# Kernel tuning notes

Measured on AMD Instinct MI355X. Metric: run time of the kernel, lower is better.

The kernel has to match this reference:

```python
import jax, jax.numpy as jnp
import numpy as np

B, S, E, L, H, FF, CB = 16, 1000, 512, 4, 8, 2048, 4096
DH = E // H

def _ln(x, g, b):
    m = x.mean(-1, keepdims=True)
    v = ((x - m) ** 2).mean(-1, keepdims=True)
    return (x - m) / jnp.sqrt(v + 1e-5) * g + b

def setup_inputs() -> dict:
    key = jax.random.key(0)
    cnt = [0]
    def rn(shape, s=0.02):
        cnt[0] += 1
        return jax.random.normal(jax.random.fold_in(key, cnt[0]), shape, jnp.float32) * s
    inp = {}
    inp['noisy_tokens'] = jax.random.randint(jax.random.fold_in(key, 999), (B, S), 0, CB, dtype=jnp.int32)
    inp['codebook'] = rn((CB, E), 1.0)
    # sinusoidal positional encoding, as in _create_positional_encoding
    pe = np.zeros((S, E), np.float32)
    pos = np.arange(S, dtype=np.float32)[:, None]
    div = np.exp(np.arange(0, E, 2, dtype=np.float32) * (-np.log(10000.0) / E))
    pe[:, 0::2] = np.sin(pos * div)
    pe[:, 1::2] = np.cos(pos * div)
    inp['pos_enc'] = jnp.asarray(pe)[None]  # [1,S,E]
    # transformer encoder layers (stacked over L)
    inp['qkv_w'] = rn((L, 3 * E, E)); inp['qkv_b'] = jnp.zeros((L, 3 * E))
    inp['out_w'] = rn((L, E, E));     inp['out_b'] = jnp.zeros((L, E))
    inp['ln1_g'] = jnp.ones((L, E));  inp['ln1_b'] = jnp.zeros((L, E))
    inp['ln2_g'] = jnp.ones((L, E));  inp['ln2_b'] = jnp.zeros((L, E))
    inp['ff1_w'] = rn((L, FF, E));    inp['ff1_b'] = jnp.zeros((L, FF))
    inp['ff2_w'] = rn((L, E, FF));    inp['ff2_b'] = jnp.zeros((L, E))
    inp['fin_g'] = jnp.ones((E,));    inp['fin_b'] = jnp.zeros((E,))
    # post_process: Linear, LN, GELU, Linear
    inp['pp1_w'] = rn((E, E)); inp['pp1_b'] = jnp.zeros((E,))
    inp['pp_ln_g'] = jnp.ones((E,)); inp['pp_ln_b'] = jnp.zeros((E,))
    inp['pp2_w'] = rn((E, E)); inp['pp2_b'] = jnp.zeros((E,))
    inp['res_w'] = jnp.float32(0.1)
    # feature_to_codebook: Linear, LN, GELU, Linear (codebook_dim == E)
    inp['fc1_w'] = rn((E, E)); inp['fc1_b'] = jnp.zeros((E,))
    inp['fc_ln_g'] = jnp.ones((E,)); inp['fc_ln_b'] = jnp.zeros((E,))
    inp['fc2_w'] = rn((E, E)); inp['fc2_b'] = jnp.zeros((E,))
    return inp

def reference(noisy_tokens, codebook, pos_enc, qkv_w, qkv_b, out_w, out_b,
              ln1_g, ln1_b, ln2_g, ln2_b, ff1_w, ff1_b, ff2_w, ff2_b,
              fin_g, fin_b, pp1_w, pp1_b, pp_ln_g, pp_ln_b, pp2_w, pp2_b,
              res_w, fc1_w, fc1_b, fc_ln_g, fc_ln_b, fc2_w, fc2_b):
    gelu = lambda z: jax.nn.gelu(z, approximate=False)
    # token embedding (codebook_projection is Identity) + positional encoding
    x = codebook[noisy_tokens] + pos_enc            # [B,S,E]
    # pre-norm transformer encoder (dropout=0 / eval)
    y = x
    for l in range(L):
        h = _ln(y, ln1_g[l], ln1_b[l])
        qkv = h @ qkv_w[l].T + qkv_b[l]             # [B,S,3E]
        q, k, v = jnp.split(qkv, 3, axis=-1)
        q = q.reshape(B, S, H, DH); k = k.reshape(B, S, H, DH); v = v.reshape(B, S, H, DH)
        scores = jnp.einsum('bqhd,bkhd->bhqk', q, k) / jnp.sqrt(jnp.float32(DH))
        attn = jax.nn.softmax(scores, axis=-1)
        ctx = jnp.einsum('bhqk,bkhd->bqhd', attn, v).reshape(B, S, E)
        y = y + (ctx @ out_w[l].T + out_b[l])
        h2 = _ln(y, ln2_g[l], ln2_b[l])
        y = y + (gelu(h2 @ ff1_w[l].T + ff1_b[l]) @ ff2_w[l].T + ff2_b[l])
    y = _ln(y, fin_g, fin_b)
    # post_process + residual
    pp = gelu(_ln(y @ pp1_w.T + pp1_b, pp_ln_g, pp_ln_b)) @ pp2_w.T + pp2_b
    enhanced = x + res_w * pp
    # feature_to_codebook
    fc = gelu(_ln(enhanced @ fc1_w.T + fc1_b, fc_ln_g, fc_ln_b)) @ fc2_w.T + fc2_b  # [B,S,E]
    # quantize: nearest neighbour in codebook (cdist + argmin)
    flat = fc.reshape(-1, E)
    d2 = (jnp.sum(flat ** 2, -1, keepdims=True)
          - 2.0 * flat @ codebook.T
          + jnp.sum(codebook ** 2, -1))            # [B*S, CB]
    tokens = jnp.argmin(d2, axis=-1).reshape(B, S)
    return fc, tokens
```

## Files before the change

### kernel.cpp

```cpp
#include <hip/hip_runtime.h>
#include <hip/hip_bf16.h>
#include <math.h>

#define NTOK 16000
#define E    512
#define FFD  2048
#define CBN  4096
#define SEQ  1000
#define NH   8
#define VLD  1008

typedef __hip_bfloat16 bf16;
typedef __attribute__((ext_vector_type(8))) short short8;
typedef __attribute__((ext_vector_type(4))) float f32x4;

__device__ __forceinline__ float gelu_f(float v) {
    return 0.5f * v * (1.0f + erff(v * 0.70710678118654752f));
}

__device__ __forceinline__ void split_store(float v, bf16* hi, bf16* lo, size_t idx) {
    bf16 h = __float2bfloat16(v);
    hi[idx] = h;
    lo[idx] = __float2bfloat16(v - __bfloat162float(h));
}

__device__ __forceinline__ void gll16(const bf16* g, short* l) {
    __builtin_amdgcn_global_load_lds((const __attribute__((address_space(1))) void*)g,
                                     (__attribute__((address_space(3))) void*)l, 16, 0, 0);
}

__device__ __forceinline__ void t2_ins(float v, int c, float& v1, int& c1, float& v2, int& c2) {
    const bool b1 = (v < v1) || (v == v1 && c < c1);
    const bool b2 = (v < v2) || (v == v2 && c < c2);
    if (b1) { v2 = v1; c2 = c1; v1 = v; c1 = c; }
    else if (b2) { v2 = v; c2 = c; }
}

__global__ __launch_bounds__(128) void embed_kernel(const int* __restrict__ tok,
                                                    const float* __restrict__ cb,
                                                    const float* __restrict__ pe,
                                                    float* __restrict__ y) {
    const int row = blockIdx.x;
    const int s = row % SEQ;
    const int t = tok[row];
    const int c = threadIdx.x * 4;
    const float4 cv = *(const float4*)(cb + (size_t)t * E + c);
    const float4 pv = *(const float4*)(pe + (size_t)s * E + c);
    *(float4*)(y + (size_t)row * E + c) =
        make_float4(cv.x + pv.x, cv.y + pv.y, cv.z + pv.z, cv.w + pv.w);
}

__global__ __launch_bounds__(256) void split_w(const float* __restrict__ src, int ld,
                                               int cols_log2, int n,
                                               bf16* __restrict__ hi, bf16* __restrict__ lo) {
    const int i = blockIdx.x * 256 + threadIdx.x;
    if (i >= n) return;
    const int r = i >> cols_log2;
    const int c = i & ((1 << cols_log2) - 1);
    const float v = src[(size_t)r * ld + c];
    split_store(v, hi, lo, i);
}

template<int GELU>
__global__ __launch_bounds__(256) void ln_planes(const float* __restrict__ in,
                                                 bf16* __restrict__ hi, bf16* __restrict__ lo,
                                                 const float* __restrict__ g,
                                                 const float* __restrict__ b) {
    const int lane = threadIdx.x & 63;
    const int row = blockIdx.x * 4 + (threadIdx.x >> 6);
    const float* p = in + (size_t)row * E;
    const float4 v0 = *(const float4*)(p + lane * 4);
    const float4 v1 = *(const float4*)(p + 256 + lane * 4);
    float sum = v0.x + v0.y + v0.z + v0.w + v1.x + v1.y + v1.z + v1.w;
    float sq = v0.x * v0.x + v0.y * v0.y + v0.z * v0.z + v0.w * v0.w
             + v1.x * v1.x + v1.y * v1.y + v1.z * v1.z + v1.w * v1.w;
#pragma unroll
    for (int m = 1; m < 64; m <<= 1) {
        sum += __shfl_xor(sum, m);
        sq += __shfl_xor(sq, m);
    }
    const float mean = sum * (1.0f / 512.0f);
    const float var = sq * (1.0f / 512.0f) - mean * mean;
    const float rstd = rsqrtf(var + 1e-5f);
    const float4 g0 = *(const float4*)(g + lane * 4);
    const float4 g1 = *(const float4*)(g + 256 + lane * 4);
    const float4 b0 = *(const float4*)(b + lane * 4);
    const float4 b1 = *(const float4*)(b + 256 + lane * 4);
    const size_t base = (size_t)row * E;
    float o;
    const float vv0[4] = {v0.x, v0.y, v0.z, v0.w};
    const float gg0[4] = {g0.x, g0.y, g0.z, g0.w};
    const float bb0[4] = {b0.x, b0.y, b0.z, b0.w};
    const float vv1[4] = {v1.x, v1.y, v1.z, v1.w};
    const float gg1[4] = {g1.x, g1.y, g1.z, g1.w};
    const float bb1[4] = {b1.x, b1.y, b1.z, b1.w};
#pragma unroll
    for (int t = 0; t < 4; ++t) {
        o = (vv0[t] - mean) * rstd * gg0[t] + bb0[t];
        if (GELU) o = gelu_f(o);
        split_store(o, hi, lo, base + lane * 4 + t);
        o = (vv1[t] - mean) * rstd * gg1[t] + bb1[t];
        if (GELU) o = gelu_f(o);
        split_store(o, hi, lo, base + 256 + lane * 4 + t);
    }
}

template<int OUT>
__global__ __launch_bounds__(256) void gemm_split(
    const bf16* __restrict__ Ah, const bf16* __restrict__ Al, int lda,
    const bf16* __restrict__ Wh, const bf16* __restrict__ Wl, int ldw,
    const float* __restrict__ bias,
    float* __restrict__ C, int ldc,
    bf16* __restrict__ Ohi, bf16* __restrict__ Olo, int ldp,
    const int* __restrict__ noisy, const float* __restrict__ cb,
    const float* __restrict__ pe, const float* __restrict__ resw,
    int K) {
    __shared__ __align__(16) short SB[2][4][128][32];
    const int tid = threadIdx.x;
    const int rowBase = blockIdx.y * 128;
    const int colBase = blockIdx.x * 128;
    const int wave = tid >> 6, lane = tid & 63;
    const int wm = (wave & 1) * 64, wn = (wave >> 1) * 64;
    const int lm = lane & 15;
    const int psl8 = ((lane >> 4) ^ ((lm >> 1) & 3)) * 8;

    const bf16* src = (wave == 0) ? Ah : (wave == 1) ? Al : (wave == 2) ? Wh : Wl;
    const int sld = (wave < 2) ? lda : ldw;
    const int srb = (wave < 2) ? rowBase : colBase;
    const int sslot = (lane & 3) ^ ((lane >> 3) & 3);
    const bf16* sp = src + (size_t)(srb + (lane >> 2)) * sld + sslot * 8;
    short* lb0 = &SB[0][wave][0][0];
    short* lb1 = &SB[1][wave][0][0];

    f32x4 acc[4][4];
#pragma unroll
    for (int i = 0; i < 4; ++i)
#pragma unroll
        for (int j = 0; j < 4; ++j)
            acc[i][j] = (f32x4){0.f, 0.f, 0.f, 0.f};

    const int nt = K >> 5;
    {
#pragma unroll
        for (int j = 0; j < 8; ++j)
            gll16(sp + (size_t)j * 16 * sld, lb0 + j * 512);
    }
    __syncthreads();
    int cur = 0;
    for (int t = 0; t < nt; ++t) {
        if (t + 1 < nt) {
            short* lb = cur ? lb0 : lb1;
            const bf16* p = sp + (t + 1) * 32;
#pragma unroll
            for (int j = 0; j < 8; ++j)
                gll16(p + (size_t)j * 16 * sld, lb + j * 512);
        }
        const short (*P)[128][32] = SB[cur];
        short8 ah[4], al[4], wh[4], wl[4];
#pragma unroll
        for (int i = 0; i < 4; ++i) {
            ah[i] = *(const short8*)&P[0][wm + i * 16 + lm][psl8];
            al[i] = *(const short8*)&P[1][wm + i * 16 + lm][psl8];
            wh[i] = *(const short8*)&P[2][wn + i * 16 + lm][psl8];
            wl[i] = *(const short8*)&P[3][wn + i * 16 + lm][psl8];
        }
#pragma unroll
        for (int i = 0; i < 4; ++i)
#pragma unroll
            for (int j = 0; j < 4; ++j)
                acc[i][j] = __builtin_amdgcn_mfma_f32_16x16x32_bf16(ah[i], wh[j], acc[i][j], 0, 0, 0);
#pragma unroll
        for (int i = 0; i < 4; ++i)
#pragma unroll
            for (int j = 0; j < 4; ++j)
                acc[i][j] = __builtin_amdgcn_mfma_f32_16x16x32_bf16(ah[i], wl[j], acc[i][j], 0, 0, 0);
#pragma unroll
        for (int i = 0; i < 4; ++i)
#pragma unroll
            for (int j = 0; j < 4; ++j)
                acc[i][j] = __builtin_amdgcn_mfma_f32_16x16x32_bf16(al[i], wh[j], acc[i][j], 0, 0, 0);
        __syncthreads();
        cur ^= 1;
    }

    float bv[4];
#pragma unroll
    for (int j = 0; j < 4; ++j)
        bv[j] = bias ? bias[colBase + wn + j * 16 + lm] : 0.f;
    float scv = 0.f;
    if (OUT == 3) scv = resw[0];
#pragma unroll
    for (int i = 0; i < 4; ++i) {
#pragma unroll
        for (int reg = 0; reg < 4; ++reg) {
            const int r = rowBase + wm + i * 16 + (lane >> 4) * 4 + reg;
            int tok = 0, srow = 0;
            if (OUT == 3) { tok = noisy[r]; srow = r % SEQ; }
#pragma unroll
            for (int j = 0; j < 4; ++j) {
                const int col = colBase + wn + j * 16 + lm;
                float v = acc[i][j][reg] + bv[j];
                if (OUT == 0) {
                    C[(size_t)r * ldc + col] = v;
                } else if (OUT == 1) {
                    float* cp = C + (size_t)r * ldc + col;
                    *cp = *cp + v;
                } else if (OUT == 2) {
                    v = gelu_f(v);
                    split_store(v, Ohi, Olo, (size_t)r * ldp + col);
                } else if (OUT == 3) {
                    const float xv = cb[(size_t)tok * E + col] + pe[(size_t)srow * E + col];
                    v = xv + scv * v;
                    split_store(v, Ohi, Olo, (size_t)r * ldp + col);
                } else if (OUT == 4) {
                    split_store(v, Ohi, Olo, (size_t)r * ldp + col);
                } else {
                    C[(size_t)r * ldc + col] = v;
                    split_store(v, Ohi, Olo, (size_t)r * ldp + col);
                }
            }
        }
    }
}

__global__ __launch_bounds__(256) void vtrans(const bf16* __restrict__ vh_src,
                                              const bf16* __restrict__ vl_src,
                                              bf16* __restrict__ vth,
                                              bf16* __restrict__ vtl) {
    __shared__ short T[64][72];
    const int tid = threadIdx.x;
    const int st = blockIdx.x;
    const int bh = blockIdx.y;
    const int b = bh >> 3, h = bh & 7;
    const int sr = tid >> 2, dq = (tid & 3) * 16;
    const int s_g = st * 64 + sr;
    const int od = tid >> 3;
    const int osq = (tid & 7) * 8;
#pragma unroll
    for (int p = 0; p < 2; ++p) {
        const short* src = (const short*)(p ? vl_src : vh_src);
        short* dst = (short*)(p ? vtl : vth);
        short8 a0 = {0, 0, 0, 0, 0, 0, 0, 0};
        short8 a1 = {0, 0, 0, 0, 0, 0, 0, 0};
        if (s_g < SEQ) {
            const short* sp = src + (size_t)(b * SEQ + s_g) * 1536 + 1024 + h * 64 + dq;
            a0 = *(const short8*)sp;
            a1 = *(const short8*)(sp + 8);
        }
        __syncthreads();
#pragma unroll
        for (int j = 0; j < 8; ++j) T[dq + j][sr] = a0[j];
#pragma unroll
        for (int j = 0; j < 8; ++j) T[dq + 8 + j][sr] = a1[j];
        __syncthreads();
        const int scol = st * 64 + osq;
        if (scol + 8 <= VLD) {
            const short8 o0 = *(const short8*)&T[od][osq];
            const short8 o1 = *(const short8*)&T[od + 32][osq];
            *(short8*)(dst + (size_t)(bh * 64 + od) * VLD + scol) = o0;
            *(short8*)(dst + (size_t)(bh * 64 + od + 32) * VLD + scol) = o1;
        }
    }
}

__global__ __launch_bounds__(256) void attn_mfma(const bf16* __restrict__ qkh,
                                                 const bf16* __restrict__ qkl,
                                                 const bf16* __restrict__ vth,
                                                 const bf16* __restrict__ vtl,
                                                 bf16* __restrict__ chi,
                                                 bf16* __restrict__ clo) {
    __shared__ short QPs[2][64][72];
    __shared__ short Ks[2][64][72];
    __shared__ short Vs[2][64][72];
    const int tid = threadIdx.x;
    const int qt = blockIdx.x, bh = blockIdx.y;
    const int b = bh >> 3, h = bh & 7;
    const int wave = tid >> 6, lane = tid & 63;
    const int lm = lane & 15, g = lane >> 4, q8 = g * 8;
    const int wq = wave * 16;
    const int r0 = tid >> 2, kq = (tid & 3) * 16;
    const short8 z = {0, 0, 0, 0, 0, 0, 0, 0};

    {
        const int q = qt * 64 + r0;
        short8 a0 = z, a1 = z, b0 = z, b1 = z;
        if (q < SEQ) {
            const size_t base = (size_t)(b * SEQ + q) * 1536 + h * 64 + kq;
            a0 = *(const short8*)((const short*)qkh + base);
            a1 = *(const short8*)((const short*)qkh + base + 8);
            b0 = *(const short8*)((const short*)qkl + base);
            b1 = *(const short8*)((const short*)qkl + base + 8);
        }
        *(short8*)&QPs[0][r0][kq] = a0; *(short8*)&QPs[0][r0][kq + 8] = a1;
        *(short8*)&QPs[1][r0][kq] = b0; *(short8*)&QPs[1][r0][kq + 8] = b1;
    }
    __syncthreads();
    short8 qfh[2], qfl[2];
#pragma unroll
    for (int t = 0; t < 2; ++t) {
        qfh[t] = *(const short8*)&QPs[0][wq + lm][t * 32 + q8];
        qfl[t] = *(const short8*)&QPs[1][wq + lm][t * 32 + q8];
    }

    float m_i[4] = {-3e38f, -3e38f, -3e38f, -3e38f};
    float l_i[4] = {0.f, 0.f, 0.f, 0.f};
    f32x4 o[4];
#pragma unroll
    for (int dt = 0; dt < 4; ++dt) o[dt] = (f32x4){0.f, 0.f, 0.f, 0.f};

    short8 ka0 = z, ka1 = z, kl0 = z, kl1 = z;
    short8 va0 = z, va1 = z, vl0 = z, vl1 = z;
    auto loadKV = [&](int kb2) {
        const int kr = kb2 + r0;
        ka0 = z; ka1 = z; kl0 = z; kl1 = z;
        if (kr < SEQ) {
            const size_t base = (size_t)(b * SEQ + kr) * 1536 + 512 + h * 64 + kq;
            ka0 = *(const short8*)((const short*)qkh + base);
            ka1 = *(const short8*)((const short*)qkh + base + 8);
            kl0 = *(const short8*)((const short*)qkl + base);
            kl1 = *(const short8*)((const short*)qkl + base + 8);
        }
        const size_t vbase = (size_t)(bh * 64 + r0) * VLD + kb2 + kq;
        va0 = z; va1 = z; vl0 = z; vl1 = z;
        if (kb2 + kq + 8 <= VLD) {
            va0 = *(const short8*)((const short*)vth + vbase);
            vl0 = *(const short8*)((const short*)vtl + vbase);
        }
        if (kb2 + kq + 16 <= VLD) {
            va1 = *(const short8*)((const short*)vth + vbase + 8);
            vl1 = *(const short8*)((const short*)vtl + vbase + 8);
        }
    };
    loadKV(0);

    for (int kb = 0; kb < SEQ; kb += 64) {
        __syncthreads();
        {
            *(short8*)&Ks[0][r0][kq] = ka0; *(short8*)&Ks[0][r0][kq + 8] = ka1;
            *(short8*)&Ks[1][r0][kq] = kl0; *(short8*)&Ks[1][r0][kq + 8] = kl1;
            *(short8*)&Vs[0][r0][kq] = va0; *(short8*)&Vs[0][r0][kq + 8] = va1;
            *(short8*)&Vs[1][r0][kq] = vl0; *(short8*)&Vs[1][r0][kq + 8] = vl1;
        }
        __syncthreads();
        if (kb + 64 < SEQ) loadKV(kb + 64);
        f32x4 sac[4];
#pragma unroll
        for (int j = 0; j < 4; ++j) sac[j] = (f32x4){0.f, 0.f, 0.f, 0.f};
#pragma unroll
        for (int t = 0; t < 2; ++t) {
#pragma unroll
            for (int j = 0; j < 4; ++j) {
                const short8 kh = *(const short8*)&Ks[0][j * 16 + lm][t * 32 + q8];
                const short8 kl = *(const short8*)&Ks[1][j * 16 + lm][t * 32 + q8];
                sac[j] = __builtin_amdgcn_mfma_f32_16x16x32_bf16(qfh[t], kh, sac[j], 0, 0, 0);
                sac[j] = __builtin_amdgcn_mfma_f32_16x16x32_bf16(qfh[t], kl, sac[j], 0, 0, 0);
                sac[j] = __builtin_amdgcn_mfma_f32_16x16x32_bf16(qfl[t], kh, sac[j], 0, 0, 0);
            }
        }
        float alpha_v[4];
#pragma unroll
        for (int reg = 0; reg < 4; ++reg) {
            float sv[4];
            float rm = -3e38f;
#pragma unroll
            for (int j = 0; j < 4; ++j) {
                const int kc = kb + j * 16 + lm;
                float s = sac[j][reg] * 0.125f;
                s = (kc < SEQ) ? s : -3e38f;
                sv[j] = s;
                rm = fmaxf(rm, s);
            }
#pragma unroll
            for (int m = 1; m < 16; m <<= 1) rm = fmaxf(rm, __shfl_xor(rm, m));
            const float mn = fmaxf(m_i[reg], rm);
            const float al = expf(m_i[reg] - mn);
            float rs = 0.f;
            const int prow = wq + g * 4 + reg;
#pragma unroll
            for (int j = 0; j < 4; ++j) {
                const float pv = expf(sv[j] - mn);
                rs += pv;
                bf16 phb = __float2bfloat16(pv);
                bf16 plb = __float2bfloat16(pv - __bfloat162float(phb));
                QPs[0][prow][j * 16 + lm] = *reinterpret_cast<short*>(&phb);
                QPs[1][prow][j * 16 + lm] = *reinterpret_cast<short*>(&plb);
            }
#pragma unroll
            for (int m = 1; m < 16; m <<= 1) rs += __shfl_xor(rs, m);
            l_i[reg] = l_i[reg] * al + rs;
            m_i[reg] = mn;
            alpha_v[reg] = al;
        }
        const f32x4 av = {alpha_v[0], alpha_v[1], alpha_v[2], alpha_v[3]};
#pragma unroll
        for (int dt = 0; dt < 4; ++dt) o[dt] *= av;
        __syncthreads();
#pragma unroll
        for (int t = 0; t < 2; ++t) {
            const short8 ph = *(const short8*)&QPs[0][wq + lm][t * 32 + q8];
            const short8 pl = *(const short8*)&QPs[1][wq + lm][t * 32 + q8];
#pragma unroll
            for (int dt = 0; dt < 4; ++dt) {
                const short8 vh = *(const short8*)&Vs[0][dt * 16 + lm][t * 32 + q8];
                const short8 vl = *(const short8*)&Vs[1][dt * 16 + lm][t * 32 + q8];
                o[dt] = __builtin_amdgcn_mfma_f32_16x16x32_bf16(ph, vh, o[dt], 0, 0, 0);
                o[dt] = __builtin_amdgcn_mfma_f32_16x16x32_bf16(ph, vl, o[dt], 0, 0, 0);
                o[dt] = __builtin_amdgcn_mfma_f32_16x16x32_bf16(pl, vh, o[dt], 0, 0, 0);
            }
        }
    }
#pragma unroll
    for (int reg = 0; reg < 4; ++reg) {
        const int q = qt * 64 + wq + g * 4 + reg;
        if (q < SEQ) {
            const float inv = 1.0f / l_i[reg];
#pragma unroll
            for (int dt = 0; dt < 4; ++dt) {
                const size_t idx = (size_t)(b * SEQ + q) * E + h * 64 + dt * 16 + lm;
                split_store(o[dt][reg] * inv, chi, clo, idx);
            }
        }
    }
}

__global__ __launch_bounds__(256) void cbnorm_kernel(const float* __restrict__ cb,
                                                     float* __restrict__ out) {
    const int lane = threadIdx.x & 63;
    const int row = blockIdx.x * 4 + (threadIdx.x >> 6);
    const float* p = cb + (size_t)row * E;
    const float4 v0 = *(const float4*)(p + lane * 4);
    const float4 v1 = *(const float4*)(p + 256 + lane * 4);
    float sq = v0.x * v0.x + v0.y * v0.y + v0.z * v0.z + v0.w * v0.w
             + v1.x * v1.x + v1.y * v1.y + v1.z * v1.z + v1.w * v1.w;
#pragma unroll
    for (int m = 1; m < 64; m <<= 1) sq += __shfl_xor(sq, m);
    if (lane == 0) out[row] = sq;
}

__global__ __launch_bounds__(256) void argmin_mfma(
    const bf16* __restrict__ Ah, const bf16* __restrict__ Al,
    const bf16* __restrict__ Wh, const bf16* __restrict__ Wl,
    const float* __restrict__ cbn, float4* __restrict__ part) {
    __shared__ __align__(16) short SB[2][4][128][32];
    float4* mrg = reinterpret_cast<float4*>(&SB[0][0][0][0]);
    const int tid = threadIdx.x;
    const int rowBase = blockIdx.y * 128;
    const int wave = tid >> 6, lane = tid & 63;
    const int wm = wave * 32;
    const int lm = lane & 15;
    const int g = lane >> 4;
    const int psl8 = (g ^ ((lm >> 1) & 3)) * 8;
    const int own_row = tid >> 1;
    const int own_half = tid & 1;

    const bf16* ssrc = (wave == 0) ? Ah : (wave == 1) ? Al : (wave == 2) ? Wh : Wl;
    const int sslot = (lane & 3) ^ ((lane >> 3) & 3);
    short* lb0 = &SB[0][wave][0][0];
    short* lb1 = &SB[1][wave][0][0];

    float rv1 = 3e38f, rv2 = 3e38f;
    int rc1 = 0x7fffffff, rc2 = 0x7fffffff;

    for (int ct = 0; ct < 4; ++ct) {
        const int colBase = blockIdx.x * 512 + ct * 128;
        const int rb = (wave < 2) ? rowBase : colBase;
        const bf16* sp = ssrc + (size_t)(rb + (lane >> 2)) * E + sslot * 8;
        f32x4 acc[2][8];
#pragma unroll
        for (int i = 0; i < 2; ++i)
#pragma unroll
            for (int j = 0; j < 8; ++j)
                acc[i][j] = (f32x4){0.f, 0.f, 0.f, 0.f};

        __syncthreads();
        {
#pragma unroll
            for (int j = 0; j < 8; ++j)
                gll16(sp + (size_t)j * 16 * E, lb0 + j * 512);
        }
        __syncthreads();
        int cur = 0;
        for (int t = 0; t < 16; ++t) {
            if (t < 15) {
                short* lb = cur ? lb0 : lb1;
                const bf16* p = sp + (t + 1) * 32;
#pragma unroll
                for (int j = 0; j < 8; ++j)
                    gll16(p + (size_t)j * 16 * E, lb + j * 512);
            }
            const short (*P)[128][32] = SB[cur];
            short8 ah[2], al2[2], wh[8], wl[8];
#pragma unroll
            for (int i = 0; i < 2; ++i) {
                ah[i]  = *(const short8*)&P[0][wm + i * 16 + lm][psl8];
                al2[i] = *(const short8*)&P[1][wm + i * 16 + lm][psl8];
            }
#pragma unroll
            for (int j = 0; j < 8; ++j) {
                wh[j] = *(const short8*)&P[2][j * 16 + lm][psl8];
                wl[j] = *(const short8*)&P[3][j * 16 + lm][psl8];
            }
#pragma unroll
            for (int i = 0; i < 2; ++i)
#pragma unroll
                for (int j = 0; j < 8; ++j)
                    acc[i][j] = __builtin_amdgcn_mfma_f32_16x16x32_bf16(ah[i], wh[j], acc[i][j], 0, 0, 0);
#pragma unroll
            for (int i = 0; i < 2; ++i)
#pragma unroll
                for (int j = 0; j < 8; ++j)
                    acc[i][j] = __builtin_amdgcn_mfma_f32_16x16x32_bf16(ah[i], wl[j], acc[i][j], 0, 0, 0);
#pragma unroll
            for (int i = 0; i < 2; ++i)
#pragma unroll
                for (int j = 0; j < 8; ++j)
                    acc[i][j] = __builtin_amdgcn_mfma_f32_16x16x32_bf16(al2[i], wh[j], acc[i][j], 0, 0, 0);
            __syncthreads();
            cur ^= 1;
        }

        float nv[8];
#pragma unroll
        for (int j = 0; j < 8; ++j) nv[j] = cbn[colBase + j * 16 + lm];
#pragma unroll
        for (int i = 0; i < 2; ++i) {
#pragma unroll
            for (int reg = 0; reg < 4; ++reg) {
                const int row_local = wm + i * 16 + g * 4 + reg;
                float v1 = 3e38f, v2 = 3e38f;
                int c1 = 0x7fffffff, c2 = 0x7fffffff;
#pragma unroll
                for (int j = 0; j < 8; ++j) {
                    const float d = nv[j] - 2.0f * acc[i][j][reg];
                    t2_ins(d, colBase + j * 16 + lm, v1, c1, v2, c2);
                }
                mrg[row_local * 16 + (lm ^ (row_local & 15))] = make_float4(v1, (float)c1, v2, (float)c2);
            }
        }
        __syncthreads();
        {
            float mv1 = 3e38f, mv2 = 3e38f;
            int mc1 = 0x7fffffff, mc2 = 0x7fffffff;
#pragma unroll
            for (int e = 0; e < 8; ++e) {
                const int cc = own_half * 8 + e;
                const float4 p = mrg[own_row * 16 + (cc ^ (own_row & 15))];
                t2_ins(p.x, (int)p.y, mv1, mc1, mv2, mc2);
                t2_ins(p.z, (int)p.w, mv1, mc1, mv2, mc2);
            }
            const float pv1 = __shfl_xor(mv1, 1); const int pc1 = __shfl_xor(mc1, 1);
            const float pv2 = __shfl_xor(mv2, 1); const int pc2 = __shfl_xor(mc2, 1);
            t2_ins(pv1, pc1, mv1, mc1, mv2, mc2);
            t2_ins(pv2, pc2, mv1, mc1, mv2, mc2);
            t2_ins(mv1, mc1, rv1, rc1, rv2, rc2);
            t2_ins(mv2, mc2, rv1, rc1, rv2, rc2);
        }
    }
    if (own_half == 0)
        part[(size_t)(rowBase + own_row) * 8 + blockIdx.x] =
            make_float4(rv1, (float)rc1, rv2, (float)rc2);
}

__global__ __launch_bounds__(256) void argmin_exact(const float4* __restrict__ part,
                                                    const float* __restrict__ fc,
                                                    const float* __restrict__ cb,
                                                    const float* __restrict__ cbn,
                                                    float* __restrict__ tokf) {
    const int wave = threadIdx.x >> 6, lane = threadIdx.x & 63;
    const int r = blockIdx.x * 4 + wave;
    float v1 = 3e38f, v2 = 3e38f;
    int c1 = 0x7fffffff, c2 = 0x7fffffff;
    if (lane < 8) {
        const float4 p = part[(size_t)r * 8 + lane];
        v1 = p.x; c1 = (int)p.y; v2 = p.z; c2 = (int)p.w;
    }
#pragma unroll
    for (int m = 1; m < 8; m <<= 1) {
        const float w1 = __shfl_xor(v1, m); const int d1i = __shfl_xor(c1, m);
        const float w2 = __shfl_xor(v2, m); const int d2i = __shfl_xor(c2, m);
        t2_ins(w1, d1i, v1, c1, v2, c2);
        t2_ins(w2, d2i, v1, c1, v2, c2);
    }
    c1 = __shfl(c1, 0);
    c2 = __shfl(c2, 0);
    const float* fr = fc + (size_t)r * E + lane * 8;
    const float* p1 = cb + (size_t)c1 * E + lane * 8;
    const float* p2 = cb + (size_t)c2 * E + lane * 8;
    float d1 = 0.f, d2 = 0.f;
#pragma unroll
    for (int j = 0; j < 8; ++j) {
        const float f = fr[j];
        d1 += f * p1[j];
        d2 += f * p2[j];
    }
#pragma unroll
    for (int m = 1; m < 64; m <<= 1) {
        d1 += __shfl_xor(d1, m);
        d2 += __shfl_xor(d2, m);
    }
    d1 = cbn[c1] - 2.0f * d1;
    d2 = cbn[c2] - 2.0f * d2;
    const int win = ((d1 < d2) || (d1 == d2 && c1 < c2)) ? c1 : c2;
    if (lane == 0) tokf[r] = (float)win;
}

extern "C" void kernel_launch(void* const* d_in, const int* in_sizes, int n_in,
                              void* d_out, int out_size, void* d_ws, size_t ws_size,
                              hipStream_t stream) {
    const int* noisy = (const int*)d_in[0];
    const float* codebook = (const float*)d_in[1];
    const float* pos_enc = (const float*)d_in[2];
    const float* qkv_w = (const float*)d_in[3];
    const float* qkv_b = (const float*)d_in[4];
    const float* out_w = (const float*)d_in[5];
    const float* out_b = (const float*)d_in[6];
    const float* ln1_g = (const float*)d_in[7];
    const float* ln1_b = (const float*)d_in[8];
    const float* ln2_g = (const float*)d_in[9];
    const float* ln2_b = (const float*)d_in[10];
    const float* ff1_w = (const float*)d_in[11];
    const float* ff1_b = (const float*)d_in[12];
    const float* ff2_w = (const float*)d_in[13];
    const float* ff2_b = (const float*)d_in[14];
    const float* fin_g = (const float*)d_in[15];
    const float* fin_b = (const float*)d_in[16];
    const float* pp1_w = (const float*)d_in[17];
    const float* pp1_b = (const float*)d_in[18];
    const float* pp_ln_g = (const float*)d_in[19];
    const float* pp_ln_b = (const float*)d_in[20];
    const float* pp2_w = (const float*)d_in[21];
    const float* pp2_b = (const float*)d_in[22];
    const float* res_w = (const float*)d_in[23];
    const float* fc1_w = (const float*)d_in[24];
    const float* fc1_b = (const float*)d_in[25];
    const float* fc_ln_g = (const float*)d_in[26];
    const float* fc_ln_b = (const float*)d_in[27];
    const float* fc2_w = (const float*)d_in[28];
    const float* fc2_b = (const float*)d_in[29];

    float* ws = (float*)d_ws;
    float* y = ws;
    float* REG = ws + 8192000;
    bf16* qkvh = (bf16*)REG;
    bf16* qkvl = qkvh + 24576000;
    bf16* mid_hi = (bf16*)REG;
    bf16* mid_lo = mid_hi + 16384000;
    float* slotA = REG;
    float* slotB = REG + 8192000;
    bf16* e_hi = (bf16*)slotA;
    bf16* e_lo = e_hi + 8192000;
    bf16* fcp2_hi = (bf16*)(REG + 16384000);
    bf16* fcp2_lo = fcp2_hi + 8192000;
    float* WV = ws + 32768000;
    bf16* vth = (bf16*)WV;
    bf16* vtl = vth + 8192 * VLD;
    bf16* wA_hi = (bf16*)WV;
    bf16* wA_lo = wA_hi + 1048576;
    bf16* wB_hi = wA_lo + 1048576;
    bf16* wB_lo = wB_hi + 1048576;
    bf16* cbh = wB_lo + 1048576;
    bf16* cbl = cbh + 2097152;
    float* cbn = slotB;
    float4* part = (float4*)(slotB + 4096);
    bf16* h_hi = (bf16*)d_out;
    bf16* h_lo = h_hi + 8192000;
    float* tokf = (float*)d_out + 8192000;

    const dim3 blk(256);
    const dim3 g512(4, 125), g1024(8, 125), g1536(12, 125);

    embed_kernel<<<dim3(NTOK), dim3(128), 0, stream>>>(noisy, codebook, pos_enc, y);

    for (int l = 0; l < 4; ++l) {
        ln_planes<0><<<dim3(4000), blk, 0, stream>>>(y, h_hi, h_lo, ln1_g + l * E, ln1_b + l * E);
        split_w<<<dim3(3072), blk, 0, stream>>>(qkv_w + (size_t)l * 1536 * E, E, 9, 1536 * E, wA_hi, wA_lo);
        gemm_split<4><<<g1536, blk, 0, stream>>>(
            h_hi, h_lo, E, wA_hi, wA_lo, E, qkv_b + (size_t)l * 1536,
            nullptr, 0, qkvh, qkvl, 1536, nullptr, nullptr, nullptr, nullptr, E);
        vtrans<<<dim3(16, 128), blk, 0, stream>>>(qkvh, qkvl, vth, vtl);
        attn_mfma<<<dim3(16, 128), blk, 0, stream>>>(qkvh, qkvl, vth, vtl, h_hi, h_lo);
        split_w<<<dim3(1024), blk, 0, stream>>>(out_w + (size_t)l * E * E, E, 9, E * E, wB_hi, wB_lo);
        gemm_split<1><<<g512, blk, 0, stream>>>(
            h_hi, h_lo, E, wB_hi, wB_lo, E, out_b + (size_t)l * E,
            y, E, nullptr, nullptr, 0, nullptr, nullptr, nullptr, nullptr, E);
        ln_planes<0><<<dim3(4000), blk, 0, stream>>>(y, h_hi, h_lo, ln2_g + l * E, ln2_b + l * E);
        split_w<<<dim3(4096), blk, 0, stream>>>(ff1_w + (size_t)l * FFD * E, E, 9, FFD * E, wA_hi, wA_lo);
        split_w<<<dim3(4096), blk, 0, stream>>>(ff2_w + (size_t)l * E * FFD, FFD, 11, E * FFD, wB_hi, wB_lo);
        for (int c = 0; c < 2; ++c) {
            gemm_split<2><<<g1024, blk, 0, stream>>>(
                h_hi, h_lo, E, wA_hi + (size_t)c * 1024 * E, wA_lo + (size_t)c * 1024 * E, E,
                ff1_b + (size_t)l * FFD + c * 1024,
                nullptr, 0, mid_hi, mid_lo, 1024, nullptr, nullptr, nullptr, nullptr, E);
            gemm_split<1><<<g512, blk, 0, stream>>>(
                mid_hi, mid_lo, 1024, wB_hi + c * 1024, wB_lo + c * 1024, FFD,
                (c == 0) ? (ff2_b + (size_t)l * E) : nullptr,
                y, E, nullptr, nullptr, 0, nullptr, nullptr, nullptr, nullptr, 1024);
        }
    }

    ln_planes<0><<<dim3(4000), blk, 0, stream>>>(y, h_hi, h_lo, fin_g, fin_b);
    split_w<<<dim3(1024), blk, 0, stream>>>(pp1_w, E, 9, E * E, wA_hi, wA_lo);
    gemm_split<0><<<g512, blk, 0, stream>>>(
        h_hi, h_lo, E, wA_hi, wA_lo, E, pp1_b,
        slotB, E, nullptr, nullptr, 0, nullptr, nullptr, nullptr, nullptr, E);
    ln_planes<1><<<dim3(4000), blk, 0, stream>>>(slotB, h_hi, h_lo, pp_ln_g, pp_ln_b);
    split_w<<<dim3(1024), blk, 0, stream>>>(pp2_w, E, 9, E * E, wB_hi, wB_lo);
    gemm_split<3><<<g512, blk, 0, stream>>>(
        h_hi, h_lo, E, wB_hi, wB_lo, E, pp2_b,
        nullptr, 0, e_hi, e_lo, E, noisy, codebook, pos_enc, res_w, E);
    split_w<<<dim3(1024), blk, 0, stream>>>(fc1_w, E, 9, E * E, wA_hi, wA_lo);
    gemm_split<0><<<g512, blk, 0, stream>>>(
        e_hi, e_lo, E, wA_hi, wA_lo, E, fc1_b,
        slotB, E, nullptr, nullptr, 0, nullptr, nullptr, nullptr, nullptr, E);
    ln_planes<1><<<dim3(4000), blk, 0, stream>>>(slotB, h_hi, h_lo, fc_ln_g, fc_ln_b);
    split_w<<<dim3(1024), blk, 0, stream>>>(fc2_w, E, 9, E * E, wB_hi, wB_lo);
    gemm_split<5><<<g512, blk, 0, stream>>>(
        h_hi, h_lo, E, wB_hi, wB_lo, E, fc2_b,
        slotA, E, fcp2_hi, fcp2_lo, E, nullptr, nullptr, nullptr, nullptr, E);

    split_w<<<dim3(8192), blk, 0, stream>>>(codebook, E, 9, CBN * E, cbh, cbl);
    cbnorm_kernel<<<dim3(1024), blk, 0, stream>>>(codebook, cbn);
    argmin_mfma<<<dim3(8, 125), blk, 0, stream>>>(fcp2_hi, fcp2_lo, cbh, cbl, cbn, part);
    argmin_exact<<<dim3(4000), blk, 0, stream>>>(part, slotA, codebook, cbn, tokf);
    hipMemcpyAsync(d_out, slotA, (size_t)8192000 * 4, hipMemcpyDeviceToDevice, stream);
}
```

Measured before the change: 3.587 ms.

## Prefetch two K-tiles ahead with vmcnt waits instead of full syncthreads

Both the split-bf16 GEMM and the codebook-distance kernel now issue global-to-LDS loads for tiles t and t+1 up front. Each iteration waits with s_waitcnt vmcnt(8), so only the older tile must have landed, rather than draining all loads with __syncthreads. The next load into the freed buffer is issued right after the post-compute barrier. This keeps one tile of global loads in flight during the MFMA work to hide memory latency. The risk is relying on hand-counted vmcnt and raw s_barrier for correctness, which could fail if the compiler emits other vector memory ops in between.

```diff
diff --git a/kernel.cpp b/kernel.cpp
--- a/kernel.cpp
+++ b/kernel.cpp
@@ -140,21 +140,21 @@
             acc[i][j] = (f32x4){0.f, 0.f, 0.f, 0.f};
 
     const int nt = K >> 5;
+#pragma unroll
+    for (int j = 0; j < 8; ++j)
+        gll16(sp + (size_t)j * 16 * sld, lb0 + j * 512);
     {
+        const bf16* p = sp + 32;
 #pragma unroll
         for (int j = 0; j < 8; ++j)
-            gll16(sp + (size_t)j * 16 * sld, lb0 + j * 512);
-    }
-    __syncthreads();
-    int cur = 0;
+            gll16(p + (size_t)j * 16 * sld, lb1 + j * 512);
+    }
     for (int t = 0; t < nt; ++t) {
-        if (t + 1 < nt) {
-            short* lb = cur ? lb0 : lb1;
-            const bf16* p = sp + (t + 1) * 32;
-#pragma unroll
-            for (int j = 0; j < 8; ++j)
-                gll16(p + (size_t)j * 16 * sld, lb + j * 512);
-        }
+        const int cur = t & 1;
+        if (t + 1 < nt) asm volatile("s_waitcnt vmcnt(8)" ::: "memory");
+        else            asm volatile("s_waitcnt vmcnt(0)" ::: "memory");
+        __builtin_amdgcn_s_barrier();
+        __builtin_amdgcn_sched_barrier(0);
         const short (*P)[128][32] = SB[cur];
         short8 ah[4], al[4], wh[4], wl[4];
 #pragma unroll
@@ -179,8 +179,14 @@
 #pragma unroll
             for (int j = 0; j < 4; ++j)
                 acc[i][j] = __builtin_amdgcn_mfma_f32_16x16x32_bf16(al[i], wh[j], acc[i][j], 0, 0, 0);
-        __syncthreads();
-        cur ^= 1;
+        __builtin_amdgcn_s_barrier();
+        if (t + 2 < nt) {
+            short* lb = cur ? lb1 : lb0;
+            const bf16* p = sp + (t + 2) * 32;
+#pragma unroll
+            for (int j = 0; j < 8; ++j)
+                gll16(p + (size_t)j * 16 * sld, lb + j * 512);
+        }
     }
 
     float bv[4];
@@ -472,22 +478,22 @@
             for (int j = 0; j < 8; ++j)
                 acc[i][j] = (f32x4){0.f, 0.f, 0.f, 0.f};
 
-        __syncthreads();
+        __builtin_amdgcn_s_barrier();
+#pragma unroll
+        for (int j = 0; j < 8; ++j)
+            gll16(sp + (size_t)j * 16 * E, lb0 + j * 512);
         {
+            const bf16* p = sp + 32;
 #pragma unroll
             for (int j = 0; j < 8; ++j)
-                gll16(sp + (size_t)j * 16 * E, lb0 + j * 512);
-        }
-        __syncthreads();
-        int cur = 0;
+                gll16(p + (size_t)j * 16 * E, lb1 + j * 512);
+        }
         for (int t = 0; t < 16; ++t) {
-            if (t < 15) {
-                short* lb = cur ? lb0 : lb1;
-                const bf16* p = sp + (t + 1) * 32;
-#pragma unroll
-                for (int j = 0; j < 8; ++j)
-                    gll16(p + (size_t)j * 16 * E, lb + j * 512);
-            }
+            const int cur = t & 1;
+            if (t < 15) asm volatile("s_waitcnt vmcnt(8)" ::: "memory");
+            else        asm volatile("s_waitcnt vmcnt(0)" ::: "memory");
+            __builtin_amdgcn_s_barrier();
+            __builtin_amdgcn_sched_barrier(0);
             const short (*P)[128][32] = SB[cur];
             short8 ah[2], al2[2], wh[8], wl[8];
 #pragma unroll
@@ -515,8 +521,14 @@
 #pragma unroll
                 for (int j = 0; j < 8; ++j)
                     acc[i][j] = __builtin_amdgcn_mfma_f32_16x16x32_bf16(al2[i], wh[j], acc[i][j], 0, 0, 0);
-            __syncthreads();
-            cur ^= 1;
+            __builtin_amdgcn_s_barrier();
+            if (t < 14) {
+                short* lb = cur ? lb1 : lb0;
+                const bf16* p = sp + (t + 2) * 32;
+#pragma unroll
+                for (int j = 0; j < 8; ++j)
+                    gll16(p + (size_t)j * 16 * E, lb + j * 512);
+            }
         }
 
         float nv[8];
```

Measured after the change: 3.503 ms. -2.3%, faster.
